# Kernel optimization log

Measured on AMD Instinct MI355X. Metric: run time of the kernel, lower is better.

Reference implementation:

```python
import jax, jax.numpy as jnp
import numpy as np

S, G, N, E = 4, 3, 20000, 320000   # seq_len, num_graphs, nodes, edges
DIN = HID = OUT = 64


def setup_inputs() -> dict:
    key = jax.random.key(0)
    ks = jax.random.split(key, 12)
    s = 0.1  # weight scale ~ Glorot-ish for d=64
    return {
        "x": jax.random.normal(ks[0], (S, G, N, DIN), jnp.float32),
        "edge_index": jax.random.randint(ks[1], (S, G, 2, E), 0, N, dtype=jnp.int32),
        "W1l": jax.random.normal(ks[2], (G, DIN, HID), jnp.float32) * s,
        "W1r": jax.random.normal(ks[3], (G, DIN, HID), jnp.float32) * s,
        "b1": jnp.zeros((G, HID), jnp.float32),
        "W2l": jax.random.normal(ks[4], (G, HID, OUT), jnp.float32) * s,
        "W2r": jax.random.normal(ks[5], (G, HID, OUT), jnp.float32) * s,
        "b2": jnp.zeros((G, OUT), jnp.float32),
        "Wih": jax.random.normal(ks[6], (4 * OUT, OUT), jnp.float32) * s,
        "Whh": jax.random.normal(ks[7], (4 * OUT, OUT), jnp.float32) * s,
        "bih": jnp.zeros((4 * OUT,), jnp.float32),
        "bhh": jnp.zeros((4 * OUT,), jnp.float32),
    }


def _sage(x, ei, Wl, Wr, b):
    # PyG SAGEConv(aggr='mean'): out = mean_{j->i}(x_j) @ Wl + x_i @ Wr + b
    src, dst = ei[0], ei[1]
    n = x.shape[0]
    msg = jax.ops.segment_sum(x[src], dst, num_segments=n)          # [N, d]
    cnt = jax.ops.segment_sum(jnp.ones((ei.shape[1], 1), x.dtype), dst, num_segments=n)
    mean = jnp.where(cnt > 0, msg / jnp.maximum(cnt, 1.0), 0.0)
    return mean @ Wl + x @ Wr + b


def _gnn(x, ei, Wl1, Wr1, bb1, Wl2, Wr2, bb2):
    h = jnp.tanh(_sage(x, ei, Wl1, Wr1, bb1))
    return jnp.tanh(_sage(h, ei, Wl2, Wr2, bb2))


def reference(x, edge_index, W1l, W1r, b1, W2l, W2r, b2, Wih, Whh, bih, bhh):
    # vmap over graphs (each graph has its own conv weights), then over timesteps
    per_graph = jax.vmap(_gnn, in_axes=(0, 0, 0, 0, 0, 0, 0, 0))
    per_seq = jax.vmap(per_graph, in_axes=(0, 0, None, None, None, None, None, None))
    h = per_seq(x, edge_index, W1l, W1r, b1, W2l, W2r, b2)          # [S, G, N, OUT]
    # torch: per timestep stack graphs [G,N,O] -> transpose -> [N,G,O]; cat over seq on dim0
    lstm_in = jnp.transpose(h, (0, 2, 1, 3)).reshape(S * N, G, OUT)  # [B, T=G, OUT]
    B = lstm_in.shape[0]

    def step(carry, xt):
        hp, cp = carry
        gates = xt @ Wih.T + hp @ Whh.T + bih + bhh                 # [B, 4*OUT]
        i, f, g, o = jnp.split(gates, 4, axis=-1)                   # torch gate order i,f,g,o
        c = jax.nn.sigmoid(f) * cp + jax.nn.sigmoid(i) * jnp.tanh(g)
        hn = jax.nn.sigmoid(o) * jnp.tanh(c)
        return (hn, c), None

    init = (jnp.zeros((B, OUT), x.dtype), jnp.zeros((B, OUT), x.dtype))
    (h_last, _), _ = jax.lax.scan(step, init, jnp.transpose(lstm_in, (1, 0, 2)))
    return h_last  # [S*N, OUT] == lstm_out[:, -1, :].squeeze()
```

## Files before the change

### kernel.cpp

```cpp
#include <hip/hip_runtime.h>
#include <math.h>

#define S 4
#define G 3
#define NN 20000
#define EE 320000
#define D 64
#define SG (S*G)

#define RGS 32
#define RNODES2 625
#define BCAP 14336
#define CHUNKA 100

#define LTILES 314
#define LTASKS (12*LTILES)
#define LPERX  (LTASKS/8)

static __device__ __forceinline__ float rcpf(float x){ return __builtin_amdgcn_rcpf(x); }
static __device__ __forceinline__ float sigmf(float x){ return rcpf(1.0f + __expf(-x)); }
static __device__ __forceinline__ float tanhf_fast(float x){
    float t = __expf(2.0f*x);
    return 1.0f - 2.0f*rcpf(t + 1.0f);
}

static __device__ __forceinline__ unsigned short f2bf(float f){
    union { float f; unsigned u; } v; v.f = f;
    unsigned r = v.u + 0x7FFF + ((v.u >> 16) & 1);
    return (unsigned short)(r >> 16);
}

typedef short bf16x8 __attribute__((ext_vector_type(8)));
typedef float f32x4  __attribute__((ext_vector_type(4)));


__global__ __launch_bounds__(256) void binA_kernel(const int* __restrict__ ei,
                                                   int* __restrict__ bcur,
                                                   int* __restrict__ bkt){
    __shared__ int wcnt[4*RGS];
    __shared__ int wb[4*RGS];
    int chunk = blockIdx.x, sg = blockIdx.y;
    int tid = threadIdx.x, w = tid >> 6;
    const int* srcp = ei + (size_t)(sg*2 + 0)*EE;
    const int* dstp = ei + (size_t)(sg*2 + 1)*EE;
    const int EPC = EE/CHUNKA;
    int start = chunk*EPC, end = start + EPC;

    for (int it = 0; it < (EPC + 1023)/1024; ++it){
        if (tid < 4*RGS) wcnt[tid] = 0;
        __syncthreads();
        int e = start + it*1024 + tid*4;
        bool valid = e < end;
        int d_[4], s_[4], r_[4], dl_[4], rk_[4];
        if (valid){
            int4 d4 = *(const int4*)&dstp[e];
            int4 s4 = *(const int4*)&srcp[e];
            d_[0]=d4.x; d_[1]=d4.y; d_[2]=d4.z; d_[3]=d4.w;
            s_[0]=s4.x; s_[1]=s4.y; s_[2]=s4.z; s_[3]=s4.w;
            #pragma unroll
            for (int j = 0; j < 4; ++j){
                int r = d_[j] / RNODES2;
                r_[j]  = r;
                dl_[j] = d_[j] - r*RNODES2;
                rk_[j] = atomicAdd(&wcnt[w*RGS + r], 1);
            }
        }
        __syncthreads();
        if (tid < RGS){
            int c0 = wcnt[0*RGS+tid], c1 = wcnt[1*RGS+tid];
            int c2 = wcnt[2*RGS+tid], c3 = wcnt[3*RGS+tid];
            int tot = c0+c1+c2+c3;
            int gb = 0;
            if (tot > 0) gb = atomicAdd(&bcur[sg*RGS + tid], tot);
            wb[0*RGS+tid] = gb;
            wb[1*RGS+tid] = gb + c0;
            wb[2*RGS+tid] = gb + c0 + c1;
            wb[3*RGS+tid] = gb + c0 + c1 + c2;
        }
        __syncthreads();
        if (valid){
            #pragma unroll
            for (int j = 0; j < 4; ++j){
                int pos = wb[w*RGS + r_[j]] + rk_[j];
                if (pos < BCAP)
                    bkt[(size_t)(sg*RGS + r_[j])*BCAP + pos] = (dl_[j] << 15) | s_[j];
            }
        }
    }
}


__global__ __launch_bounds__(256) void buildB_kernel(int* __restrict__ bkt,
                                                     const int* __restrict__ bcur,
                                                     int* __restrict__ off2,
                                                     int* __restrict__ deg2){
    __shared__ int hist[RNODES2];
    __shared__ int pref[RNODES2];
    __shared__ int seg[BCAP];
    __shared__ int sums[256];
    int sg = blockIdx.x / RGS, rg = blockIdx.x % RGS;
    int tid = threadIdx.x;
    int cnt = bcur[sg*RGS + rg];
    if (cnt > BCAP) cnt = BCAP;
    size_t base = (size_t)(sg*RGS + rg)*BCAP;

    for (int i = tid; i < RNODES2; i += 256) hist[i] = 0;
    __syncthreads();
    for (int j = tid; j < cnt; j += 256)
        atomicAdd(&hist[bkt[base + j] >> 15], 1);
    __syncthreads();

    int lo = tid*3, hi = min(lo+3, RNODES2);
    int s = 0;
    for (int i = lo; i < hi; ++i) s += (hist[i] + 3) & ~3;
    sums[tid] = s; __syncthreads();
    for (int ofs = 1; ofs < 256; ofs <<= 1){
        int v = (tid >= ofs) ? sums[tid-ofs] : 0;
        __syncthreads();
        sums[tid] += v;
        __syncthreads();
    }
    int run = sums[tid] - s;
    int gnode = sg*NN + rg*RNODES2;
    for (int i = lo; i < hi; ++i){
        pref[i] = run;
        off2[gnode + i] = (int)base + run;
        deg2[gnode + i] = hist[i];
        run += (hist[i] + 3) & ~3;
    }
    __syncthreads();

    for (int j = tid; j < cnt; j += 256){
        int p = bkt[base + j];
        int slot = atomicAdd(&pref[p >> 15], 1);
        if (slot < BCAP) seg[slot] = p & 0x7FFF;
    }
    __syncthreads();

    int padtot = min(sums[255], BCAP);
    for (int j = tid; j < padtot; j += 256) bkt[base + j] = seg[j];
}


__global__ __launch_bounds__(256) void convert_kernel(const float* __restrict__ x,
                                                      unsigned short* __restrict__ xb){
    int idx = blockIdx.x*256 + threadIdx.x;
    if (idx >= SG*NN*16) return;
    float4 v = ((const float4*)x)[idx];
    uint2 pk;
    pk.x = (unsigned)f2bf(v.x) | ((unsigned)f2bf(v.y) << 16);
    pk.y = (unsigned)f2bf(v.z) | ((unsigned)f2bf(v.w) << 16);
    ((uint2*)xb)[idx] = pk;
}


__global__ __launch_bounds__(256) void wprep2_kernel(const float* __restrict__ W1l,
                                                     const float* __restrict__ W1r,
                                                     const float* __restrict__ W2l,
                                                     const float* __restrict__ W2r,
                                                     const float* __restrict__ Wih,
                                                     const float* __restrict__ Whh,
                                                     const float* __restrict__ bih,
                                                     const float* __restrict__ bhh,
                                                     unsigned short* __restrict__ WL1,
                                                     unsigned short* __restrict__ WL2,
                                                     unsigned short* __restrict__ Wt,
                                                     float* __restrict__ bc){
    int idx = blockIdx.x*256 + threadIdx.x;
    if (idx < 24576){
        int g = idx >> 13, rem = idx & 8191, col = rem >> 7, k = rem & 127;
        float v = (k < 64) ? W1l[((size_t)g*64 + k)*64 + col]
                           : W1r[((size_t)g*64 + (k-64))*64 + col];
        WL1[idx] = f2bf(v);
    } else if (idx < 49152){
        int t = idx - 24576;
        int g = t >> 13, rem = t & 8191, col = rem >> 7, k = rem & 127;
        float v = (k < 64) ? W2l[((size_t)g*64 + k)*64 + col]
                           : W2r[((size_t)g*64 + (k-64))*64 + col];
        WL2[t] = f2bf(v);
    } else if (idx < 81920){
        int t = idx - 49152;
        int col = t >> 7, k = t & 127;
        float v = (k < 64) ? Wih[col*64 + k] : Whh[col*64 + (k - 64)];
        Wt[t] = f2bf(v);
    } else if (idx < 82176){
        int t = idx - 81920;
        bc[t] = bih[t] + bhh[t];
    }
}


#define WP 72

__global__ __launch_bounds__(256,3) void layer_kernel(const unsigned short* __restrict__ xb,
                                                    const int* __restrict__ off2,
                                                    const int* __restrict__ deg2,
                                                    const int* __restrict__ csr,
                                                    const unsigned short* __restrict__ WL,
                                                    const float* __restrict__ bias,
                                                    unsigned short* __restrict__ outb){
    __shared__ unsigned short sO[4][16*WP];
    int L = blockIdx.x;
    int xcd = L & 7, k = L >> 3;
    int task = xcd*LPERX + k;
    int sg = task / LTILES;
    int tile = task - sg*LTILES;
    if (tile >= (NN + 63)/64) return;
    int g = sg % G;
    int tid = threadIdx.x;
    int row0 = tile*64;
    const unsigned short* inb = xb + (size_t)sg*NN*D;
    const char* inbc = (const char*)inb;

    int wave = tid >> 6, lane = tid & 63;
    int i0 = row0 + wave*16;
    int r = lane & 15, q = lane >> 4;
    unsigned qb = (unsigned)(q << 4);

    const unsigned short* WLg = WL + (size_t)g*64*128;
    bf16x8 B0[4], B1[4];
    #pragma unroll
    for (int ct = 0; ct < 4; ++ct){
        B0[ct] = *(const bf16x8*)&WLg[(ct*16 + r)*128 + 0*32 + q*8];
        B1[ct] = *(const bf16x8*)&WLg[(ct*16 + r)*128 + 1*32 + q*8];
    }

    int i = i0 + r;
    int dg = 0, a = 0;
    if (i < NN){ a = off2[sg*NN + i]; dg = deg2[sg*NN + i]; }
    int mx = dg;
    mx = max(mx, __shfl_xor(mx, 1));
    mx = max(mx, __shfl_xor(mx, 2));
    mx = max(mx, __shfl_xor(mx, 4));
    mx = max(mx, __shfl_xor(mx, 8));

    int irow = min(i, NN-1);
    bf16x8 S0 = *(const bf16x8*)(inbc + (((unsigned)irow) << 7) + qb);
    bf16x8 S1 = *(const bf16x8*)(inbc + (((unsigned)irow) << 7) + qb + 64);

    unsigned zoff = (((unsigned)((SG - sg)*NN)) << 7) + qb;

    f32x4 acc[4];
    #pragma unroll
    for (int ct = 0; ct < 4; ++ct) acc[ct] = (f32x4){0.f,0.f,0.f,0.f};

    if (mx > 0){
        int4 ix = *(const int4*)&csr[a];
        bf16x8 A0[4], A1[4];
        {
            int ii[4] = {ix.x, ix.y, ix.z, ix.w};
            #pragma unroll
            for (int j = 0; j < 4; ++j){
                unsigned off = (((unsigned)ii[j]) << 7) + qb;
                if (j >= dg) off = zoff;
                A0[j] = *(const bf16x8*)(inbc + off);
                A1[j] = *(const bf16x8*)(inbc + off + 64);
            }
        }
        int4 ixn = *(const int4*)&csr[a + 4];
        for (int s4 = 0; s4 < mx; s4 += 4){
            bf16x8 N0[4], N1[4];
            {
                int ii[4] = {ixn.x, ixn.y, ixn.z, ixn.w};
                #pragma unroll
                for (int j = 0; j < 4; ++j){
                    unsigned off = (((unsigned)ii[j]) << 7) + qb;
                    if (s4 + 4 + j >= dg) off = zoff;
                    N0[j] = *(const bf16x8*)(inbc + off);
                    N1[j] = *(const bf16x8*)(inbc + off + 64);
                }
            }
            ixn = *(const int4*)&csr[a + s4 + 8];
            __builtin_amdgcn_s_setprio(1);
            #pragma unroll
            for (int j = 0; j < 4; ++j){
                #pragma unroll
                for (int ct = 0; ct < 4; ++ct)
                    acc[ct] = __builtin_amdgcn_mfma_f32_16x16x32_bf16(A0[j], B0[ct], acc[ct], 0, 0, 0);
                #pragma unroll
                for (int ct = 0; ct < 4; ++ct)
                    acc[ct] = __builtin_amdgcn_mfma_f32_16x16x32_bf16(A1[j], B1[ct], acc[ct], 0, 0, 0);
            }
            __builtin_amdgcn_s_setprio(0);
            #pragma unroll
            for (int j = 0; j < 4; ++j){ A0[j] = N0[j]; A1[j] = N1[j]; }
        }
    }

    float inv[4];
    #pragma unroll
    for (int reg = 0; reg < 4; ++reg){
        int d = __shfl(dg, (q << 2) | reg, 16);
        inv[reg] = (d > 0) ? rcpf((float)d) : 0.0f;
    }
    #pragma unroll
    for (int ct = 0; ct < 4; ++ct)
        #pragma unroll
        for (int reg = 0; reg < 4; ++reg)
            acc[ct][reg] *= inv[reg];

    #pragma unroll
    for (int ct = 0; ct < 4; ++ct){
        bf16x8 b2 = *(const bf16x8*)&WLg[(ct*16 + r)*128 + 2*32 + q*8];
        acc[ct] = __builtin_amdgcn_mfma_f32_16x16x32_bf16(S0, b2, acc[ct], 0, 0, 0);
        bf16x8 b3 = *(const bf16x8*)&WLg[(ct*16 + r)*128 + 3*32 + q*8];
        acc[ct] = __builtin_amdgcn_mfma_f32_16x16x32_bf16(S1, b3, acc[ct], 0, 0, 0);
    }

    #pragma unroll
    for (int ct = 0; ct < 4; ++ct){
        float bv = bias[g*64 + ct*16 + r];
        #pragma unroll
        for (int reg = 0; reg < 4; ++reg)
            sO[wave][(q*4+reg)*WP + ct*16 + r] = f2bf(tanhf_fast(acc[ct][reg] + bv));
    }
    #pragma unroll
    for (int pass = 0; pass < 2; ++pass){
        int rloc = pass*8 + (lane >> 3), chunk = lane & 7;
        int i2 = i0 + rloc;
        if (i2 < NN){
            uint4 v = *(const uint4*)&sO[wave][rloc*WP + chunk*8];
            *(uint4*)&outb[((size_t)sg*NN + i2)*D + chunk*8] = v;
        }
    }
}


__global__ __launch_bounds__(256) void lstm_kernel(const unsigned short* __restrict__ h2b,
                                                   const unsigned short* __restrict__ Wt,
                                                   const float* __restrict__ bc,
                                                   float* __restrict__ out){
    __shared__ unsigned short sH[64*WP];
    int tid = threadIdx.x;
    int b0 = blockIdx.x * 64;
    int wave = tid >> 6, lane = tid & 63;
    int n0 = lane & 15, q = lane >> 4;
    int jcol = wave*16 + n0;

    float bb[4];
    #pragma unroll
    for (int T = 0; T < 4; ++T) bb[T] = bc[T*64 + jcol];

    float c[4][4];
    #pragma unroll
    for (int rt = 0; rt < 4; ++rt)
        #pragma unroll
        for (int reg = 0; reg < 4; ++reg) c[rt][reg] = 0.0f;

    int s_[4], n_[4];
    #pragma unroll
    for (int rt = 0; rt < 4; ++rt){
        int b = b0 + rt*16 + n0;
        s_[rt] = b / NN; n_[rt] = b - s_[rt]*NN;
    }

    #pragma unroll
    for (int t = 0; t < G; ++t){
        f32x4 accv[4][4];
        #pragma unroll
        for (int rt = 0; rt < 4; ++rt)
            #pragma unroll
            for (int T = 0; T < 4; ++T) accv[rt][T] = (f32x4){0.f,0.f,0.f,0.f};

        int nkc = (t == 0) ? 2 : 4;
        #pragma unroll
        for (int kc = 0; kc < 4; ++kc){
            if (kc >= nkc) break;
            bf16x8 af[4];
            #pragma unroll
            for (int rt = 0; rt < 4; ++rt){
                if (kc < 2) af[rt] = *(const bf16x8*)&h2b[((size_t)(s_[rt]*G + t)*NN + n_[rt])*D + kc*32 + q*8];
                else        af[rt] = *(const bf16x8*)&sH[(rt*16 + n0)*WP + (kc-2)*32 + q*8];
            }
            #pragma unroll
            for (int T = 0; T < 4; ++T){
                int ct = T*4 + wave;
                bf16x8 bfr = *(const bf16x8*)&Wt[(ct*16 + n0)*128 + kc*32 + q*8];
                #pragma unroll
                for (int rt = 0; rt < 4; ++rt)
                    accv[rt][T] = __builtin_amdgcn_mfma_f32_16x16x32_bf16(af[rt], bfr, accv[rt][T], 0, 0, 0);
            }
        }
        if (t > 0) __syncthreads();

        #pragma unroll
        for (int rt = 0; rt < 4; ++rt){
            #pragma unroll
            for (int reg = 0; reg < 4; ++reg){
                float ig = sigmf(accv[rt][0][reg] + bb[0]);
                float fg = sigmf(accv[rt][1][reg] + bb[1]);
                float gg = tanhf_fast(accv[rt][2][reg] + bb[2]);
                float og = sigmf(accv[rt][3][reg] + bb[3]);
                float cn = fg*c[rt][reg] + ig*gg;
                c[rt][reg] = cn;
                float hv = og * tanhf_fast(cn);
                int row = rt*16 + q*4 + reg;
                if (t < G-1) sH[row*WP + jcol] = f2bf(hv);
                else         out[(size_t)(b0 + row)*D + jcol] = hv;
            }
        }
        if (t < G-1) __syncthreads();
    }
}


extern "C" void kernel_launch(void* const* d_in, const int* in_sizes, int n_in,
                              void* d_out, int out_size, void* d_ws, size_t ws_size,
                              hipStream_t stream) {
    const float* x   = (const float*)d_in[0];
    const int*   ei  = (const int*)  d_in[1];
    const float* W1l = (const float*)d_in[2];
    const float* W1r = (const float*)d_in[3];
    const float* b1  = (const float*)d_in[4];
    const float* W2l = (const float*)d_in[5];
    const float* W2r = (const float*)d_in[6];
    const float* b2  = (const float*)d_in[7];
    const float* Wih = (const float*)d_in[8];
    const float* Whh = (const float*)d_in[9];
    const float* bih = (const float*)d_in[10];
    const float* bhh = (const float*)d_in[11];
    float* out = (float*)d_out;

    char* ws = (char*)d_ws;
    size_t cur = 0;
    auto alloc = [&](size_t bytes)->void*{
        cur = (cur + 255) & ~(size_t)255;
        void* p = ws + cur; cur += bytes; return p;
    };
    int*   bkt  = (int*)alloc((size_t)SG*RGS*BCAP*4);
    int*   bcur = (int*)alloc((size_t)SG*RGS*4);
    int*   off2 = (int*)alloc((size_t)SG*NN*4);
    int*   deg2 = (int*)alloc((size_t)SG*NN*4);
    unsigned short* xb  = (unsigned short*)alloc(((size_t)SG*NN + 1)*D*2);
    unsigned short* h1b = (unsigned short*)alloc(((size_t)SG*NN + 1)*D*2);
    unsigned short* h2b = (unsigned short*)alloc((size_t)SG*NN*D*2);
    unsigned short* WL1 = (unsigned short*)alloc((size_t)G*64*128*2);
    unsigned short* WL2 = (unsigned short*)alloc((size_t)G*64*128*2);
    unsigned short* Wt  = (unsigned short*)alloc((size_t)256*128*2);
    float* bc   = (float*)alloc((size_t)256*4);
    (void)ws_size; (void)in_sizes; (void)n_in; (void)out_size;

    (void)hipMemsetAsync(bcur, 0, (size_t)SG*RGS*4, stream);
    (void)hipMemsetAsync(xb  + (size_t)SG*NN*D, 0, (size_t)D*2, stream);
    (void)hipMemsetAsync(h1b + (size_t)SG*NN*D, 0, (size_t)D*2, stream);

    convert_kernel<<<(SG*NN*16 + 255)/256, 256, 0, stream>>>(x, xb);
    binA_kernel  <<<dim3(CHUNKA, SG), 256, 0, stream>>>(ei, bcur, bkt);
    buildB_kernel<<<SG*RGS, 256, 0, stream>>>(bkt, bcur, off2, deg2);
    wprep2_kernel<<<321, 256, 0, stream>>>(W1l, W1r, W2l, W2r, Wih, Whh, bih, bhh,
                                           WL1, WL2, Wt, bc);

    layer_kernel<<<LTASKS, 256, 0, stream>>>(xb,  off2, deg2, bkt, WL1, b1, h1b);
    layer_kernel<<<LTASKS, 256, 0, stream>>>(h1b, off2, deg2, bkt, WL2, b2, h2b);

    lstm_kernel <<<(S*NN)/64, 256, 0, stream>>>(h2b, Wt, bc, out);
}
```

Before: 462.2 us.

## Sort nodes by degree per bucket and deepen gather prefetch pipeline

buildB now counting-sorts the nodes of each 625-node range by in-degree and writes permuted off/deg arrays plus a node-id map. The layer kernel then groups nodes of similar degree into each 16-row MFMA tile, which cuts the padded iterations driven by the per-tile max degree, and scatters its output through the id map. The gather loop also moves from a double-buffered 4-neighbour chunk to a triple-buffered ring of three chunks with deeper index prefetch. Launch bounds drop from 3 to 2 waves per SIMD to make room for the extra registers, which costs occupancy, and the output writes become scattered.

```diff
diff --git a/kernel.cpp b/kernel.cpp
--- a/kernel.cpp
+++ b/kernel.cpp
@@ -93,18 +93,23 @@
 __global__ __launch_bounds__(256) void buildB_kernel(int* __restrict__ bkt,
                                                      const int* __restrict__ bcur,
                                                      int* __restrict__ off2,
-                                                     int* __restrict__ deg2){
+                                                     int* __restrict__ deg2,
+                                                     int* __restrict__ nid2,
+                                                     int* __restrict__ offU){
     __shared__ int hist[RNODES2];
     __shared__ int pref[RNODES2];
     __shared__ int seg[BCAP];
     __shared__ int sums[256];
+    __shared__ int dh[64];
     int sg = blockIdx.x / RGS, rg = blockIdx.x % RGS;
     int tid = threadIdx.x;
     int cnt = bcur[sg*RGS + rg];
     if (cnt > BCAP) cnt = BCAP;
     size_t base = (size_t)(sg*RGS + rg)*BCAP;
+    int gnode = sg*NN + rg*RNODES2;
 
     for (int i = tid; i < RNODES2; i += 256) hist[i] = 0;
+    if (tid < 64) dh[tid] = 0;
     __syncthreads();
     for (int j = tid; j < cnt; j += 256)
         atomicAdd(&hist[bkt[base + j] >> 15], 1);
@@ -121,12 +126,26 @@
         __syncthreads();
     }
     int run = sums[tid] - s;
-    int gnode = sg*NN + rg*RNODES2;
     for (int i = lo; i < hi; ++i){
         pref[i] = run;
-        off2[gnode + i] = (int)base + run;
-        deg2[gnode + i] = hist[i];
+        offU[gnode + i] = (int)base + run;
         run += (hist[i] + 3) & ~3;
+    }
+    __syncthreads();
+
+    for (int i = tid; i < RNODES2; i += 256)
+        atomicAdd(&dh[min(hist[i], 63)], 1);
+    __syncthreads();
+    if (tid == 0){
+        int r = 0;
+        for (int k = 0; k < 64; ++k){ int c = dh[k]; dh[k] = r; r += c; }
+    }
+    __syncthreads();
+    for (int i = tid; i < RNODES2; i += 256){
+        int pos = atomicAdd(&dh[min(hist[i], 63)], 1);
+        off2[gnode + pos] = offU[gnode + i];
+        deg2[gnode + pos] = hist[i];
+        nid2[gnode + pos] = rg*RNODES2 + i;
     }
     __syncthreads();
 
@@ -192,9 +211,38 @@
 
 #define WP 72
 
-__global__ __launch_bounds__(256,3) void layer_kernel(const unsigned short* __restrict__ xb,
+#define LOADCH(F, IX, JB) { \
+    int ii0_ = (IX).x, ii1_ = (IX).y, ii2_ = (IX).z, ii3_ = (IX).w; \
+    unsigned o0_ = (((unsigned)ii0_) << 7) + qb; if ((JB) + 0 >= dg) o0_ = zoff; \
+    unsigned o1_ = (((unsigned)ii1_) << 7) + qb; if ((JB) + 1 >= dg) o1_ = zoff; \
+    unsigned o2_ = (((unsigned)ii2_) << 7) + qb; if ((JB) + 2 >= dg) o2_ = zoff; \
+    unsigned o3_ = (((unsigned)ii3_) << 7) + qb; if ((JB) + 3 >= dg) o3_ = zoff; \
+    F[0] = *(const bf16x8*)(inbc + o0_); F[1] = *(const bf16x8*)(inbc + o0_ + 64); \
+    F[2] = *(const bf16x8*)(inbc + o1_); F[3] = *(const bf16x8*)(inbc + o1_ + 64); \
+    F[4] = *(const bf16x8*)(inbc + o2_); F[5] = *(const bf16x8*)(inbc + o2_ + 64); \
+    F[6] = *(const bf16x8*)(inbc + o3_); F[7] = *(const bf16x8*)(inbc + o3_ + 64); \
+}
+
+#define STEP(F, IX, C) { \
+    __builtin_amdgcn_s_setprio(1); \
+    _Pragma("unroll") \
+    for (int j_ = 0; j_ < 4; ++j_){ \
+        _Pragma("unroll") \
+        for (int ct_ = 0; ct_ < 4; ++ct_) \
+            acc[ct_] = __builtin_amdgcn_mfma_f32_16x16x32_bf16(F[2*j_],   B0[ct_], acc[ct_], 0, 0, 0); \
+        _Pragma("unroll") \
+        for (int ct_ = 0; ct_ < 4; ++ct_) \
+            acc[ct_] = __builtin_amdgcn_mfma_f32_16x16x32_bf16(F[2*j_+1], B1[ct_], acc[ct_], 0, 0, 0); \
+    } \
+    __builtin_amdgcn_s_setprio(0); \
+    LOADCH(F, IX, ((C)+3)*4); \
+    IX = *(const int4*)&csr[a + ((C)+6)*4]; \
+}
+
+__global__ __launch_bounds__(256,2) void layer_kernel(const unsigned short* __restrict__ xb,
                                                     const int* __restrict__ off2,
                                                     const int* __restrict__ deg2,
+                                                    const int* __restrict__ nid2,
                                                     const int* __restrict__ csr,
                                                     const unsigned short* __restrict__ WL,
                                                     const float* __restrict__ bias,
@@ -226,17 +274,20 @@
     }
 
     int i = i0 + r;
-    int dg = 0, a = 0;
-    if (i < NN){ a = off2[sg*NN + i]; dg = deg2[sg*NN + i]; }
+    int node = 0, dg = 0, a = 0;
+    if (i < NN){
+        node = nid2[sg*NN + i];
+        a    = off2[sg*NN + i];
+        dg   = deg2[sg*NN + i];
+    }
     int mx = dg;
     mx = max(mx, __shfl_xor(mx, 1));
     mx = max(mx, __shfl_xor(mx, 2));
     mx = max(mx, __shfl_xor(mx, 4));
     mx = max(mx, __shfl_xor(mx, 8));
 
-    int irow = min(i, NN-1);
-    bf16x8 S0 = *(const bf16x8*)(inbc + (((unsigned)irow) << 7) + qb);
-    bf16x8 S1 = *(const bf16x8*)(inbc + (((unsigned)irow) << 7) + qb + 64);
+    bf16x8 S0 = *(const bf16x8*)(inbc + (((unsigned)node) << 7) + qb);
+    bf16x8 S1 = *(const bf16x8*)(inbc + (((unsigned)node) << 7) + qb + 64);
 
     unsigned zoff = (((unsigned)((SG - sg)*NN)) << 7) + qb;
 
@@ -245,45 +296,21 @@
     for (int ct = 0; ct < 4; ++ct) acc[ct] = (f32x4){0.f,0.f,0.f,0.f};
 
     if (mx > 0){
-        int4 ix = *(const int4*)&csr[a];
-        bf16x8 A0[4], A1[4];
-        {
-            int ii[4] = {ix.x, ix.y, ix.z, ix.w};
-            #pragma unroll
-            for (int j = 0; j < 4; ++j){
-                unsigned off = (((unsigned)ii[j]) << 7) + qb;
-                if (j >= dg) off = zoff;
-                A0[j] = *(const bf16x8*)(inbc + off);
-                A1[j] = *(const bf16x8*)(inbc + off + 64);
-            }
-        }
-        int4 ixn = *(const int4*)&csr[a + 4];
-        for (int s4 = 0; s4 < mx; s4 += 4){
-            bf16x8 N0[4], N1[4];
-            {
-                int ii[4] = {ixn.x, ixn.y, ixn.z, ixn.w};
-                #pragma unroll
-                for (int j = 0; j < 4; ++j){
-                    unsigned off = (((unsigned)ii[j]) << 7) + qb;
-                    if (s4 + 4 + j >= dg) off = zoff;
-                    N0[j] = *(const bf16x8*)(inbc + off);
-                    N1[j] = *(const bf16x8*)(inbc + off + 64);
-                }
-            }
-            ixn = *(const int4*)&csr[a + s4 + 8];
-            __builtin_amdgcn_s_setprio(1);
-            #pragma unroll
-            for (int j = 0; j < 4; ++j){
-                #pragma unroll
-                for (int ct = 0; ct < 4; ++ct)
-                    acc[ct] = __builtin_amdgcn_mfma_f32_16x16x32_bf16(A0[j], B0[ct], acc[ct], 0, 0, 0);
-                #pragma unroll
-                for (int ct = 0; ct < 4; ++ct)
-                    acc[ct] = __builtin_amdgcn_mfma_f32_16x16x32_bf16(A1[j], B1[ct], acc[ct], 0, 0, 0);
-            }
-            __builtin_amdgcn_s_setprio(0);
-            #pragma unroll
-            for (int j = 0; j < 4; ++j){ A0[j] = N0[j]; A1[j] = N1[j]; }
+        int4 ix0 = *(const int4*)&csr[a];
+        int4 ix1 = *(const int4*)&csr[a + 4];
+        int4 ix2 = *(const int4*)&csr[a + 8];
+        bf16x8 F0[8], F1[8], F2[8];
+        LOADCH(F0, ix0, 0);
+        LOADCH(F1, ix1, 4);
+        LOADCH(F2, ix2, 8);
+        ix0 = *(const int4*)&csr[a + 12];
+        ix1 = *(const int4*)&csr[a + 16];
+        ix2 = *(const int4*)&csr[a + 20];
+        int nch = (mx + 3) >> 2;
+        for (int c = 0; c < nch; c += 3){
+            STEP(F0, ix0, c);
+            if (c + 1 < nch) STEP(F1, ix1, c + 1);
+            if (c + 2 < nch) STEP(F2, ix2, c + 2);
         }
     }
 
@@ -319,8 +346,9 @@
         int rloc = pass*8 + (lane >> 3), chunk = lane & 7;
         int i2 = i0 + rloc;
         if (i2 < NN){
+            int nd = nid2[sg*NN + i2];
             uint4 v = *(const uint4*)&sO[wave][rloc*WP + chunk*8];
-            *(uint4*)&outb[((size_t)sg*NN + i2)*D + chunk*8] = v;
+            *(uint4*)&outb[((size_t)sg*NN + nd)*D + chunk*8] = v;
         }
     }
 }
@@ -431,6 +459,8 @@
     int*   bcur = (int*)alloc((size_t)SG*RGS*4);
     int*   off2 = (int*)alloc((size_t)SG*NN*4);
     int*   deg2 = (int*)alloc((size_t)SG*NN*4);
+    int*   nid2 = (int*)alloc((size_t)SG*NN*4);
+    int*   offU = (int*)alloc((size_t)SG*NN*4);
     unsigned short* xb  = (unsigned short*)alloc(((size_t)SG*NN + 1)*D*2);
     unsigned short* h1b = (unsigned short*)alloc(((size_t)SG*NN + 1)*D*2);
     unsigned short* h2b = (unsigned short*)alloc((size_t)SG*NN*D*2);
@@ -446,12 +476,12 @@
 
     convert_kernel<<<(SG*NN*16 + 255)/256, 256, 0, stream>>>(x, xb);
     binA_kernel  <<<dim3(CHUNKA, SG), 256, 0, stream>>>(ei, bcur, bkt);
-    buildB_kernel<<<SG*RGS, 256, 0, stream>>>(bkt, bcur, off2, deg2);
+    buildB_kernel<<<SG*RGS, 256, 0, stream>>>(bkt, bcur, off2, deg2, nid2, offU);
     wprep2_kernel<<<321, 256, 0, stream>>>(W1l, W1r, W2l, W2r, Wih, Whh, bih, bhh,
                                            WL1, WL2, Wt, bc);
 
-    layer_kernel<<<LTASKS, 256, 0, stream>>>(xb,  off2, deg2, bkt, WL1, b1, h1b);
-    layer_kernel<<<LTASKS, 256, 0, stream>>>(h1b, off2, deg2, bkt, WL2, b2, h2b);
+    layer_kernel<<<LTASKS, 256, 0, stream>>>(xb,  off2, deg2, nid2, bkt, WL1, b1, h1b);
+    layer_kernel<<<LTASKS, 256, 0, stream>>>(h1b, off2, deg2, nid2, bkt, WL2, b2, h2b);
 
     lstm_kernel <<<(S*NN)/64, 256, 0, stream>>>(h2b, Wt, bc, out);
 }
```

After: 475.2 us. 1.03x slower.
